# Kernel tuning notes

Hardware: AMD Instinct MI355X
Metric: run time of the kernel (lower is better)

## Reference

```python
import jax, jax.numpy as jnp
import numpy as np

N_NODES = 100000
N_EDGES = 1600000
N_GRAPHS = 128
ATOM_F = 92
BOND_F = 41
EMB = 64
HID = 128
CHG = 16
N_LAYERS = 3
EPS = 1e-5


def setup_inputs() -> dict:
    key = jax.random.key(0)
    ks = jax.random.split(key, 32)
    s = 0.05
    inp = {
        "x": jax.random.normal(ks[0], (N_NODES, ATOM_F), jnp.float32),
        "edge_attr": jax.random.uniform(ks[1], (N_EDGES, BOND_F), jnp.float32),
        "charge": jax.random.normal(ks[2], (N_GRAPHS,), jnp.float32),
        "edge_index": jax.random.randint(ks[3], (2, N_EDGES), 0, N_NODES),
        "batch": jnp.sort(jax.random.randint(ks[4], (N_NODES,), 0, N_GRAPHS)),
        # embeddings
        "W_charge": jax.random.normal(ks[5], (1, CHG), jnp.float32) * s,
        "b_charge": jnp.zeros((CHG,), jnp.float32),
        "W_atom": jax.random.normal(ks[6], (ATOM_F + CHG, EMB), jnp.float32) * s,
        "b_atom": jnp.zeros((EMB,), jnp.float32),
        "W_bond": jax.random.normal(ks[7], (BOND_F, EMB), jnp.float32) * s,
        "b_bond": jnp.zeros((EMB,), jnp.float32),
        # conv layers (stacked over layer dim)
        "conv_eW1": jax.random.normal(ks[8], (N_LAYERS, 3 * EMB, EMB), jnp.float32) * s,
        "conv_eb1": jnp.zeros((N_LAYERS, EMB), jnp.float32),
        "conv_eW2": jax.random.normal(ks[9], (N_LAYERS, EMB, EMB), jnp.float32) * s,
        "conv_eb2": jnp.zeros((N_LAYERS, EMB), jnp.float32),
        "conv_nW1": jax.random.normal(ks[10], (N_LAYERS, 2 * EMB, EMB), jnp.float32) * s,
        "conv_nb1": jnp.zeros((N_LAYERS, EMB), jnp.float32),
        "conv_nW2": jax.random.normal(ks[11], (N_LAYERS, EMB, EMB), jnp.float32) * s,
        "conv_nb2": jnp.zeros((N_LAYERS, EMB), jnp.float32),
        "bn_gamma": jnp.ones((N_LAYERS, EMB), jnp.float32),
        "bn_beta": jnp.zeros((N_LAYERS, EMB), jnp.float32),
        # predictor
        "pW1": jax.random.normal(ks[12], (EMB, HID), jnp.float32) * s,
        "pb1": jnp.zeros((HID,), jnp.float32),
        "pW2": jax.random.normal(ks[13], (HID, HID), jnp.float32) * s,
        "pb2": jnp.zeros((HID,), jnp.float32),
        "pW3": jax.random.normal(ks[14], (HID, 1), jnp.float32) * s,
        "pb3": jnp.zeros((1,), jnp.float32),
    }
    return inp


def reference(x, edge_attr, charge, W_charge, b_charge, W_atom, b_atom,
              W_bond, b_bond, conv_eW1, conv_eb1, conv_eW2, conv_eb2,
              conv_nW1, conv_nb1, conv_nW2, conv_nb2, bn_gamma, bn_beta,
              pW1, pb1, pW2, pb2, pW3, pb3, edge_index, batch):
    sp = jax.nn.softplus
    n_nodes = x.shape[0]
    n_graphs = charge.shape[0]

    # early charge integration: per-graph charge embedding broadcast to nodes
    charge_feat = charge[:, None] @ W_charge + b_charge          # [B, CHG]
    x = jnp.concatenate([x, charge_feat[batch]], axis=1)          # [N, ATOM_F+CHG]
    x = x @ W_atom + b_atom                                       # [N, EMB]
    ea = edge_attr @ W_bond + b_bond                              # [E, EMB]

    row, col = edge_index[0], edge_index[1]
    for i in range(conv_eW1.shape[0]):
        xr, xc = x[row], x[col]                                   # gathers [E, EMB]
        # edge update: MLP on [x_row, x_col, edge_attr]
        e_in = jnp.concatenate([xr, xc, ea], axis=1)              # [E, 3*EMB]
        ea = sp(e_in @ conv_eW1[i] + conv_eb1[i]) @ conv_eW2[i] + conv_eb2[i]
        # node messages: MLP on [x_row, new edge_attr]
        m_in = jnp.concatenate([xr, ea], axis=1)                  # [E, 2*EMB]
        msg = sp(m_in @ conv_nW1[i] + conv_nb1[i]) @ conv_nW2[i] + conv_nb2[i]
        x_new = jax.ops.segment_sum(msg, col, num_segments=n_nodes)
        # BatchNorm1d (training-mode batch stats, biased variance)
        mean = jnp.mean(x_new, axis=0)
        var = jnp.var(x_new, axis=0)
        x_new = (x_new - mean) * jax.lax.rsqrt(var + EPS) * bn_gamma[i] + bn_beta[i]
        x = sp(x_new) + x                                         # residual

    # global mean pool over graphs
    sums = jax.ops.segment_sum(x, batch, num_segments=n_graphs)   # [B, EMB]
    cnt = jax.ops.segment_sum(jnp.ones((n_nodes, 1), x.dtype), batch, num_segments=n_graphs)
    g = sums / jnp.maximum(cnt, 1.0)

    # predictor MLP (dropout is identity in eval mode)
    h = sp(g @ pW1 + pb1)
    h = sp(h @ pW2 + pb2)
    out = h @ pW3 + pb3                                           # [B, 1]
    return out.squeeze(-1)
```

## Files before the change

kernel.cpp:

```cpp
#include <hip/hip_runtime.h>
#include <math.h>

typedef short v8s __attribute__((ext_vector_type(8)));
typedef float v4f __attribute__((ext_vector_type(4)));

__device__ __forceinline__ float sp_f(float x) {
  return fmaxf(x, 0.0f) + 0.69314718056f * __log2f(1.0f + __expf(-fabsf(x)));
}

__device__ __forceinline__ unsigned short f2bf(float f) {
  union { float f; unsigned u; } x; x.f = f;
  unsigned r = (x.u + 0x7FFF + ((x.u >> 16) & 1)) >> 16;
  return (unsigned short)r;
}

__device__ __forceinline__ float bf2f(unsigned short h) {
  union { unsigned u; float f; } x; x.u = ((unsigned)h) << 16;
  return x.f;
}

__global__ __launch_bounds__(256) void k_prep_wfrag(
    const float* __restrict__ eW1, const float* __restrict__ eW2,
    const float* __restrict__ nW1, const float* __restrict__ nW2,
    unsigned short* __restrict__ wfrag) {
  int i = blockIdx.x >> 2;
  int m = blockIdx.x & 3;
  const float* W;
  if (m == 0)      W = eW1 + (size_t)i * 192 * 64 + 128 * 64;
  else if (m == 1) W = eW2 + (size_t)i * 64 * 64;
  else if (m == 2) W = nW1 + (size_t)i * 128 * 64 + 64 * 64;
  else             W = nW2 + (size_t)i * 64 * 64;
  unsigned short* out = wfrag + ((size_t)i * 4 + m) * 4096;
  for (int f = threadIdx.x; f < 4096; f += 256) {
    int j = f & 7, ln = (f >> 3) & 63, kh = (f >> 9) & 1, ct = f >> 10;
    int k = kh * 32 + (ln >> 4) * 8 + j;
    int n = ct * 16 + (ln & 15);
    out[f] = f2bf(W[k * 64 + n]);
  }
}

__global__ __launch_bounds__(256) void k_embed_nodes(
    const float* __restrict__ x, const int* __restrict__ batch,
    const float* __restrict__ charge, const float* __restrict__ W_charge,
    const float* __restrict__ b_charge, const float* __restrict__ W_atom,
    const float* __restrict__ b_atom, float* __restrict__ xemb, int N) {
  __shared__ float sW[108 * 64];
  __shared__ float sX[128 * 92];
  __shared__ float sb[64];
  __shared__ float sWc[16];
  __shared__ float sbc[16];
  for (int i = threadIdx.x; i < 108 * 64; i += blockDim.x) sW[i] = W_atom[i];
  if (threadIdx.x < 64) sb[threadIdx.x] = b_atom[threadIdx.x];
  if (threadIdx.x < 16) {
    sWc[threadIdx.x] = W_charge[threadIdx.x];
    sbc[threadIdx.x] = b_charge[threadIdx.x];
  }
  int ntiles = (N + 127) >> 7;
  for (int tile = blockIdx.x; tile < ntiles; tile += gridDim.x) {
    int base = tile << 7;
    int cnt = N - base; if (cnt > 128) cnt = 128;
    __syncthreads();
    if (cnt == 128) {
      const float4* src = (const float4*)(x + (size_t)base * 92);
      for (int i = threadIdx.x; i < 2944; i += 256) ((float4*)sX)[i] = src[i];
    } else {
      for (int i = threadIdx.x; i < cnt * 92; i += 256)
        sX[i] = x[(size_t)base * 92 + i];
    }
    __syncthreads();
    int t = threadIdx.x;
    int node = t & 127, half = t >> 7;
    if (node < cnt) {
      int n = base + node;
      float acc[32];
#pragma unroll
      for (int j = 0; j < 32; ++j) acc[j] = sb[half * 32 + j];
      const float* xr = sX + node * 92;
      for (int k = 0; k < 92; ++k) {
        float a = xr[k];
        const float* wk = sW + k * 64 + half * 32;
#pragma unroll
        for (int j = 0; j < 32; ++j) acc[j] = fmaf(a, wk[j], acc[j]);
      }
      float ch = charge[batch[n]];
#pragma unroll
      for (int c = 0; c < 16; ++c) {
        float cf = fmaf(ch, sWc[c], sbc[c]);
        const float* wk = sW + (92 + c) * 64 + half * 32;
#pragma unroll
        for (int j = 0; j < 32; ++j) acc[j] = fmaf(cf, wk[j], acc[j]);
      }
      float* o = xemb + (size_t)n * 64 + half * 32;
#pragma unroll
      for (int q8 = 0; q8 < 8; ++q8)
        ((float4*)o)[q8] = make_float4(acc[4*q8], acc[4*q8+1], acc[4*q8+2], acc[4*q8+3]);
    }
  }
}

__global__ __launch_bounds__(256) void k_hist(const int* __restrict__ col,
                                              int* __restrict__ counts, int E) {
  int stride = gridDim.x * blockDim.x;
  for (int e = blockIdx.x * blockDim.x + threadIdx.x; e < E; e += stride)
    atomicAdd(&counts[col[e]], 1);
}

__global__ __launch_bounds__(256) void k_scan1(const int* __restrict__ counts,
                                               int* __restrict__ scan_tmp,
                                               int* __restrict__ bsum, int N) {
  __shared__ int sd[2][256];
  int t = threadIdx.x;
  int i = blockIdx.x * 256 + t;
  int v = (i < N) ? counts[i] : 0;
  sd[0][t] = v;
  __syncthreads();
  int s = 0;
#pragma unroll
  for (int off = 1; off < 256; off <<= 1) {
    int nv = sd[s][t];
    if (t >= off) nv += sd[s][t - off];
    sd[s ^ 1][t] = nv;
    s ^= 1;
    __syncthreads();
  }
  if (i < N) scan_tmp[i] = sd[s][t];
  if (t == 255) bsum[blockIdx.x] = sd[s][255];
}

__global__ __launch_bounds__(256) void k_scan2(int* __restrict__ b, int NB) {
  __shared__ int sd[2][256];
  __shared__ int carry_s;
  int t = threadIdx.x;
  if (t == 0) carry_s = 0;
  __syncthreads();
  for (int base = 0; base < NB; base += 256) {
    int i = base + t;
    int v = (i < NB) ? b[i] : 0;
    sd[0][t] = v;
    __syncthreads();
    int s = 0;
#pragma unroll
    for (int off = 1; off < 256; off <<= 1) {
      int nv = sd[s][t];
      if (t >= off) nv += sd[s][t - off];
      sd[s ^ 1][t] = nv;
      s ^= 1;
      __syncthreads();
    }
    int c = carry_s;
    int tot = sd[s][255];
    if (i < NB) b[i] = sd[s][t] + c;
    __syncthreads();
    if (t == 0) carry_s = c + tot;
    __syncthreads();
  }
}

__global__ __launch_bounds__(256) void k_scan3(const int* __restrict__ counts,
                                               const int* __restrict__ scan_tmp,
                                               const int* __restrict__ bsum,
                                               int* __restrict__ cursor, int N) {
  int i = blockIdx.x * 256 + threadIdx.x;
  if (i < N) {
    int base = (blockIdx.x > 0) ? bsum[blockIdx.x - 1] : 0;
    cursor[i] = scan_tmp[i] - counts[i] + base;
  }
}

__global__ __launch_bounds__(256) void k_scatter(
    const int* __restrict__ row, const int* __restrict__ col,
    int* __restrict__ cursor, int* __restrict__ pos,
    int* __restrict__ row_s, int* __restrict__ col_s, int E) {
  int stride = gridDim.x * blockDim.x;
  for (int e = blockIdx.x * blockDim.x + threadIdx.x; e < E; e += stride) {
    int c = col[e];
    int p = atomicAdd(&cursor[c], 1);
    pos[e] = p;
    row_s[p] = row[e];
    col_s[p] = c;
  }
}

__global__ __launch_bounds__(256) void k_embed_bonds_pos(
    const float* __restrict__ eattr, const int* __restrict__ pos,
    const float* __restrict__ W_bond, const float* __restrict__ b_bond,
    unsigned short* __restrict__ ea16, int E) {
  __shared__ float sW[41 * 64];
  __shared__ float sE[256 * 41];
  __shared__ float sb[64];
  for (int i = threadIdx.x; i < 41 * 64; i += blockDim.x) sW[i] = W_bond[i];
  if (threadIdx.x < 64) sb[threadIdx.x] = b_bond[threadIdx.x];
  int ntiles = (E + 255) >> 8;
  for (int tile = blockIdx.x; tile < ntiles; tile += gridDim.x) {
    int base = tile << 8;
    int cnt = E - base; if (cnt > 256) cnt = 256;
    __syncthreads();
    if (cnt == 256) {
      const float4* src = (const float4*)(eattr + (size_t)base * 41);
      for (int i = threadIdx.x; i < 2624; i += 256) ((float4*)sE)[i] = src[i];
    } else {
      for (int i = threadIdx.x; i < cnt * 41; i += 256)
        sE[i] = eattr[(size_t)base * 41 + i];
    }
    __syncthreads();
    int t = threadIdx.x;
    if (t < cnt) {
      float acc[64];
#pragma unroll
      for (int j = 0; j < 64; ++j) acc[j] = sb[j];
      const float* er = sE + t * 41;
      for (int k = 0; k < 41; ++k) {
        float a = er[k];
        const float* wk = sW + k * 64;
#pragma unroll
        for (int j = 0; j < 64; ++j) acc[j] = fmaf(a, wk[j], acc[j]);
      }
      size_t ob = (size_t)pos[base + t] * 64;
#pragma unroll
      for (int q8 = 0; q8 < 8; ++q8) {
        unsigned short tmp[8];
#pragma unroll
        for (int j = 0; j < 8; ++j) tmp[j] = f2bf(acc[q8 * 8 + j]);
        *(uint4*)&ea16[ob + q8 * 8] = *(uint4*)tmp;
      }
    }
  }
}

__device__ __forceinline__ void node_pre_body(
    const float* __restrict__ xr, const float* sWa, const float* sWb,
    const float* sWp, unsigned short* __restrict__ up16,
    unsigned short* __restrict__ v16, int n) {
  const float4* xr4 = (const float4*)xr;
  float u[64], p[64];
#pragma unroll
  for (int j = 0; j < 64; ++j) { u[j] = 0.f; p[j] = 0.f; }
  for (int k4 = 0; k4 < 16; ++k4) {
    float4 av = xr4[k4];
    const float* wa = sWa + k4 * 256;
    const float* wp = sWp + k4 * 256;
#pragma unroll
    for (int j = 0; j < 64; ++j) u[j] = fmaf(av.x, wa[j], u[j]);
#pragma unroll
    for (int j = 0; j < 64; ++j) p[j] = fmaf(av.x, wp[j], p[j]);
#pragma unroll
    for (int j = 0; j < 64; ++j) u[j] = fmaf(av.y, wa[64 + j], u[j]);
#pragma unroll
    for (int j = 0; j < 64; ++j) p[j] = fmaf(av.y, wp[64 + j], p[j]);
#pragma unroll
    for (int j = 0; j < 64; ++j) u[j] = fmaf(av.z, wa[128 + j], u[j]);
#pragma unroll
    for (int j = 0; j < 64; ++j) p[j] = fmaf(av.z, wp[128 + j], p[j]);
#pragma unroll
    for (int j = 0; j < 64; ++j) u[j] = fmaf(av.w, wa[192 + j], u[j]);
#pragma unroll
    for (int j = 0; j < 64; ++j) p[j] = fmaf(av.w, wp[192 + j], p[j]);
  }
  unsigned short* o = up16 + (size_t)n * 128;
#pragma unroll
  for (int q8 = 0; q8 < 8; ++q8) {
    unsigned short tmp[8];
#pragma unroll
    for (int j = 0; j < 8; ++j) {
      int i = q8 * 8 + j;
      tmp[j] = f2bf(u[((i & 3) << 4) | (i >> 2)]);
    }
    *(uint4*)&o[q8 * 8] = *(uint4*)tmp;
  }
#pragma unroll
  for (int q8 = 0; q8 < 8; ++q8) {
    unsigned short tmp[8];
#pragma unroll
    for (int j = 0; j < 8; ++j) {
      int i = q8 * 8 + j;
      tmp[j] = f2bf(p[((i & 3) << 4) | (i >> 2)]);
    }
    *(uint4*)&o[64 + q8 * 8] = *(uint4*)tmp;
  }
  float vv[64];
#pragma unroll
  for (int j = 0; j < 64; ++j) vv[j] = 0.f;
  for (int k4 = 0; k4 < 16; ++k4) {
    float4 av = xr4[k4];
    const float* wb = sWb + k4 * 256;
#pragma unroll
    for (int j = 0; j < 64; ++j) vv[j] = fmaf(av.x, wb[j], vv[j]);
#pragma unroll
    for (int j = 0; j < 64; ++j) vv[j] = fmaf(av.y, wb[64 + j], vv[j]);
#pragma unroll
    for (int j = 0; j < 64; ++j) vv[j] = fmaf(av.z, wb[128 + j], vv[j]);
#pragma unroll
    for (int j = 0; j < 64; ++j) vv[j] = fmaf(av.w, wb[192 + j], vv[j]);
  }
  unsigned short* ov = v16 + (size_t)n * 64;
#pragma unroll
  for (int q8 = 0; q8 < 8; ++q8) {
    unsigned short tmp[8];
#pragma unroll
    for (int j = 0; j < 8; ++j) {
      int i = q8 * 8 + j;
      tmp[j] = f2bf(vv[((i & 3) << 4) | (i >> 2)]);
    }
    *(uint4*)&ov[q8 * 8] = *(uint4*)tmp;
  }
}

__global__ __launch_bounds__(256) void k_node_pre(
    const float* __restrict__ xemb, const float* __restrict__ eW1,
    const float* __restrict__ nW1, unsigned short* __restrict__ up16,
    unsigned short* __restrict__ v16, int N) {
  __shared__ float sWa[64 * 64];
  __shared__ float sWb[64 * 64];
  __shared__ float sWp[64 * 64];
  for (int i = threadIdx.x; i < 64 * 64; i += blockDim.x) {
    sWa[i] = eW1[i];
    sWb[i] = eW1[64 * 64 + i];
    sWp[i] = nW1[i];
  }
  __syncthreads();
  int stride = gridDim.x * blockDim.x;
  for (int n = blockIdx.x * blockDim.x + threadIdx.x; n < N; n += stride)
    node_pre_body(xemb + (size_t)n * 64, sWa, sWb, sWp, up16, v16, n);
}

__global__ __launch_bounds__(256) void k_bn_pre(
    float* __restrict__ xemb, const float* __restrict__ xnew,
    const float* __restrict__ bnacc, const float* __restrict__ gamma,
    const float* __restrict__ beta, const float* __restrict__ eW1n,
    const float* __restrict__ nW1n, unsigned short* __restrict__ up16,
    unsigned short* __restrict__ v16, int N) {
  __shared__ float sWa[64 * 64];
  __shared__ float sWb[64 * 64];
  __shared__ float sWp[64 * 64];
  __shared__ float sscale[64], sshift[64];
  for (int i = threadIdx.x; i < 64 * 64; i += blockDim.x) {
    sWa[i] = eW1n[i];
    sWb[i] = eW1n[64 * 64 + i];
    sWp[i] = nW1n[i];
  }
  if (threadIdx.x < 64) {
    float inv = 1.0f / (float)N;
    float m = bnacc[threadIdx.x] * inv;
    float var = bnacc[64 + threadIdx.x] * inv - m * m;
    float rs = rsqrtf(var + 1e-5f);
    float g = gamma[threadIdx.x];
    sscale[threadIdx.x] = rs * g;
    sshift[threadIdx.x] = beta[threadIdx.x] - m * rs * g;
  }
  __syncthreads();
  int stride = gridDim.x * blockDim.x;
  for (int n = blockIdx.x * blockDim.x + threadIdx.x; n < N; n += stride) {
    float* xr = xemb + (size_t)n * 64;
#pragma unroll
    for (int q = 0; q < 16; ++q) {
      float4 xn4 = ((const float4*)(xnew + (size_t)n * 64))[q];
      float4 xo4 = ((const float4*)xr)[q];
      xo4.x += sp_f(fmaf(xn4.x, sscale[4*q+0], sshift[4*q+0]));
      xo4.y += sp_f(fmaf(xn4.y, sscale[4*q+1], sshift[4*q+1]));
      xo4.z += sp_f(fmaf(xn4.z, sscale[4*q+2], sshift[4*q+2]));
      xo4.w += sp_f(fmaf(xn4.w, sscale[4*q+3], sshift[4*q+3]));
      ((float4*)xr)[q] = xo4;
    }
    node_pre_body(xr, sWa, sWb, sWp, up16, v16, n);
  }
}

#define READ_FRAGS(P)                                                        \
  {                                                                          \
    const v8s* wp_ = (const v8s*)gWf + (P) * 512;                            \
    _Pragma("unroll") for (int ct = 0; ct < 4; ++ct)                         \
        _Pragma("unroll") for (int kh = 0; kh < 2; ++kh)                     \
            bfr[ct][kh] = wp_[(ct * 2 + kh) * 64 + l];                       \
    _Pragma("unroll") for (int rb = 0; rb < 2; ++rb)                         \
        _Pragma("unroll") for (int kh = 0; kh < 2; ++kh) {                   \
      int row_ = rbase + rb * 16 + c16;                                      \
      af[rb][kh] = *(const v8s*)&sA[row_ * 64 +                              \
                                    ((kh * 32 + q * 8) ^ ((row_ & 7) << 3))];\
    }                                                                        \
  }

#define DO_MFMA()                                                            \
  _Pragma("unroll") for (int rb = 0; rb < 2; ++rb)                           \
      _Pragma("unroll") for (int ct = 0; ct < 4; ++ct) {                     \
    v4f a_ = {0.f, 0.f, 0.f, 0.f};                                           \
    a_ = __builtin_amdgcn_mfma_f32_16x16x32_bf16(af[rb][0], bfr[ct][0], a_,  \
                                                 0, 0, 0);                   \
    a_ = __builtin_amdgcn_mfma_f32_16x16x32_bf16(af[rb][1], bfr[ct][1], a_,  \
                                                 0, 0, 0);                   \
    acc[rb][ct] = a_;                                                        \
  }

__global__ __launch_bounds__(256, 4) void k_edge_mfma(
    const int* __restrict__ row_s, const int* __restrict__ col_s,
    unsigned short* __restrict__ ea16, const unsigned short* __restrict__ up16,
    const unsigned short* __restrict__ v16,
    const unsigned short* __restrict__ gWf, const float* __restrict__ eb1,
    const float* __restrict__ eb2, const float* __restrict__ nb1,
    const float* __restrict__ nb2, float* __restrict__ xnew, int E) {
  __shared__ __align__(16) unsigned char smem[34304];
  unsigned short* sA = (unsigned short*)smem;
  float* msgb        = (float*)smem;
  float* sBb         = (float*)(smem + 32768);
  int* scol          = (int*)(smem + 33792);

  int tid = threadIdx.x;
  int te = blockIdx.x * 128;
  int w = tid >> 6, l = tid & 63, q = l >> 4, c16 = l & 15;
  int rbase = w * 32;

  int rid[2][4], cid[2][4], eid[2][4];
#pragma unroll
  for (int rb = 0; rb < 2; ++rb)
#pragma unroll
    for (int r = 0; r < 4; ++r) {
      int rit = rbase + rb * 16 + q * 4 + r;
      int e = te + rit;
      eid[rb][r] = e;
      int ec = e < E ? e : E - 1;
      rid[rb][r] = row_s[ec];
      cid[rb][r] = col_s[ec];
    }
  ushort4 uu_pf[2][4], vv_pf[2][4];
#pragma unroll
  for (int rb = 0; rb < 2; ++rb)
#pragma unroll
    for (int r = 0; r < 4; ++r) {
      uu_pf[rb][r] = *(const ushort4*)&up16[(size_t)rid[rb][r] * 128 + c16 * 4];
      vv_pf[rb][r] = *(const ushort4*)&v16[(size_t)cid[rb][r] * 64 + c16 * 4];
    }

  if (tid < 64) {
    sBb[0 * 64 + tid] = eb1[tid];
    sBb[1 * 64 + tid] = eb2[tid];
    sBb[2 * 64 + tid] = nb1[tid];
    sBb[3 * 64 + tid] = nb2[tid];
  }
  if (tid < 128) {
    int e = te + tid;
    scol[tid] = col_s[e < E ? e : E - 1];
  }
  for (int i = tid; i < 1024; i += 256) {
    int r = i >> 3, cc = i & 7;
    int e = te + r;
    if (e >= E) e = E - 1;
    uint4 d = *(const uint4*)&ea16[(size_t)e * 64 + cc * 8];
    *(uint4*)&sA[r * 64 + ((cc * 8) ^ ((r & 7) << 3))] = d;
  }

  v8s af[2][2];
  v8s bfr[4][2];
  v4f acc[2][4];

  __syncthreads();

  READ_FRAGS(0);
  DO_MFMA();
  ushort4 pp_pf[2][4];
#pragma unroll
  for (int rb = 0; rb < 2; ++rb)
#pragma unroll
    for (int r = 0; r < 4; ++r)
      pp_pf[rb][r] =
          *(const ushort4*)&up16[(size_t)rid[rb][r] * 128 + 64 + c16 * 4];
#pragma unroll
  for (int rb = 0; rb < 2; ++rb)
#pragma unroll
    for (int r = 0; r < 4; ++r) {
      int row = rbase + rb * 16 + q * 4 + r;
      const unsigned short* up_ = (const unsigned short*)&uu_pf[rb][r];
      const unsigned short* vp_ = (const unsigned short*)&vv_pf[rb][r];
#pragma unroll
      for (int ct = 0; ct < 4; ++ct) {
        int n = ct * 16 + c16;
        float t = acc[rb][ct][r] + sBb[n] + bf2f(up_[ct]) + bf2f(vp_[ct]);
        t = sp_f(t);
        sA[row * 64 + (n ^ ((row & 7) << 3))] = f2bf(t);
      }
    }

  READ_FRAGS(1);
  DO_MFMA();
#pragma unroll
  for (int rb = 0; rb < 2; ++rb)
#pragma unroll
    for (int ct = 0; ct < 4; ++ct) {
      int n = ct * 16 + c16;
#pragma unroll
      for (int r = 0; r < 4; ++r) {
        float en = acc[rb][ct][r] + sBb[64 + n];
        int row = rbase + rb * 16 + q * 4 + r;
        sA[row * 64 + (n ^ ((row & 7) << 3))] = f2bf(en);
      }
    }
  __syncthreads();
  for (int i = tid; i < 1024; i += 256) {
    int r = i >> 3, cc = i & 7;
    if (te + r < E) {
      uint4 d = *(const uint4*)&sA[r * 64 + ((cc * 8) ^ ((r & 7) << 3))];
      *(uint4*)&ea16[(size_t)(te + r) * 64 + cc * 8] = d;
    }
  }
  __syncthreads();

  READ_FRAGS(2);
  DO_MFMA();
#pragma unroll
  for (int rb = 0; rb < 2; ++rb)
#pragma unroll
    for (int r = 0; r < 4; ++r) {
      int row = rbase + rb * 16 + q * 4 + r;
      const unsigned short* pp_ = (const unsigned short*)&pp_pf[rb][r];
#pragma unroll
      for (int ct = 0; ct < 4; ++ct) {
        int n = ct * 16 + c16;
        float t2 = acc[rb][ct][r] + sBb[128 + n] + bf2f(pp_[ct]);
        t2 = sp_f(t2);
        sA[row * 64 + (n ^ ((row & 7) << 3))] = f2bf(t2);
      }
    }

  READ_FRAGS(3);
  __syncthreads();
  DO_MFMA();
#pragma unroll
  for (int rb = 0; rb < 2; ++rb)
#pragma unroll
    for (int ct = 0; ct < 4; ++ct) {
      int n = ct * 16 + c16;
#pragma unroll
      for (int r = 0; r < 4; ++r) {
        float msg = acc[rb][ct][r] + sBb[192 + n];
        int row = rbase + rb * 16 + q * 4 + r;
        msgb[row * 64 + n] = (eid[rb][r] < E) ? msg : 0.0f;
      }
    }
  __syncthreads();

  int nrows = E - te;
  if (nrows > 128) nrows = 128;
  for (int r0 = w; r0 < nrows; r0 += 4) {
    int c0 = scol[r0];
    if (r0 > 0 && scol[r0 - 1] == c0) continue;
    float s = 0.0f;
    int r = r0;
    do {
      s += msgb[r * 64 + l];
      ++r;
    } while (r < nrows && scol[r] == c0);
    atomicAdd(&xnew[(size_t)c0 * 64 + l], s);
  }
}

__global__ __launch_bounds__(256) void k_bn_stats(
    const float* __restrict__ xnew, float* __restrict__ bnacc, int N) {
  int t = threadIdx.x;
  int ch = t & 63;
  int sl = t >> 6;
  float s = 0.f, s2 = 0.f;
  for (int n = blockIdx.x * 4 + sl; n < N; n += gridDim.x * 4) {
    float v = xnew[(size_t)n * 64 + ch];
    s += v;
    s2 = fmaf(v, v, s2);
  }
  __shared__ float red[256], red2[256];
  red[t] = s;
  red2[t] = s2;
  __syncthreads();
  if (sl == 0) {
    s = red[ch] + red[64 + ch] + red[128 + ch] + red[192 + ch];
    s2 = red2[ch] + red2[64 + ch] + red2[128 + ch] + red2[192 + ch];
    atomicAdd(&bnacc[ch], s);
    atomicAdd(&bnacc[64 + ch], s2);
  }
}

__global__ __launch_bounds__(256) void k_bn_apply(
    float* __restrict__ x, const float* __restrict__ xnew,
    const float* __restrict__ bnacc, const float* __restrict__ gamma,
    const float* __restrict__ beta, int N) {
  __shared__ float sscale[64], sshift[64];
  if (threadIdx.x < 64) {
    float inv = 1.0f / (float)N;
    float m = bnacc[threadIdx.x] * inv;
    float var = bnacc[64 + threadIdx.x] * inv - m * m;
    float rs = rsqrtf(var + 1e-5f);
    float g = gamma[threadIdx.x];
    sscale[threadIdx.x] = rs * g;
    sshift[threadIdx.x] = beta[threadIdx.x] - m * rs * g;
  }
  __syncthreads();
  size_t total = (size_t)N * 64;
  size_t stride = (size_t)gridDim.x * blockDim.x;
  for (size_t i = (size_t)blockIdx.x * blockDim.x + threadIdx.x; i < total; i += stride) {
    int ch = (int)(i & 63);
    float v = fmaf(xnew[i], sscale[ch], sshift[ch]);
    x[i] += sp_f(v);
  }
}

__device__ __forceinline__ int lbound(const int* a, int n, int key) {
  int lo = 0, hi = n;
  while (lo < hi) {
    int mid = (lo + hi) >> 1;
    if (a[mid] < key) lo = mid + 1; else hi = mid;
  }
  return lo;
}

__global__ __launch_bounds__(256) void k_pool_pred(
    const float* __restrict__ x, const int* __restrict__ batch, int N,
    const float* __restrict__ pW1, const float* __restrict__ pb1,
    const float* __restrict__ pW2, const float* __restrict__ pb2,
    const float* __restrict__ pW3, const float* __restrict__ pb3,
    float* __restrict__ out) {
  int b = blockIdx.x;
  int lo = lbound(batch, N, b);
  int hi = lbound(batch, N, b + 1);
  int t = threadIdx.x;
  int ch = t & 63;
  int sl = t >> 6;
  float s = 0.f;
  for (int n = lo + sl; n < hi; n += 4) s += x[(size_t)n * 64 + ch];
  __shared__ float red4[4][64];
  __shared__ float sg[64];
  __shared__ float sh1[128];
  __shared__ float red[128];
  red4[sl][ch] = s;
  __syncthreads();
  if (t < 64) {
    float tot = red4[0][t] + red4[1][t] + red4[2][t] + red4[3][t];
    float cnt = (float)(hi - lo);
    sg[t] = tot / fmaxf(cnt, 1.0f);
  }
  __syncthreads();
  if (t < 128) {
    float h = pb1[t];
    for (int k = 0; k < 64; ++k) h = fmaf(sg[k], pW1[k * 128 + t], h);
    sh1[t] = sp_f(h);
  }
  __syncthreads();
  if (t < 128) {
    float h = pb2[t];
    for (int k = 0; k < 128; ++k) h = fmaf(sh1[k], pW2[k * 128 + t], h);
    red[t] = sp_f(h) * pW3[t];
  }
  __syncthreads();
  for (int off = 64; off > 0; off >>= 1) {
    if (t < off) red[t] += red[t + off];
    __syncthreads();
  }
  if (t == 0) out[b] = red[0] + pb3[0];
}

extern "C" void kernel_launch(void* const* d_in, const int* in_sizes, int n_in,
                              void* d_out, int out_size, void* d_ws, size_t ws_size,
                              hipStream_t stream) {
  const float* x         = (const float*)d_in[0];
  const float* edge_attr = (const float*)d_in[1];
  const float* charge    = (const float*)d_in[2];
  const int*   eidx      = (const int*)d_in[3];
  const int*   batch     = (const int*)d_in[4];
  const float* W_charge  = (const float*)d_in[5];
  const float* b_charge  = (const float*)d_in[6];
  const float* W_atom    = (const float*)d_in[7];
  const float* b_atom    = (const float*)d_in[8];
  const float* W_bond    = (const float*)d_in[9];
  const float* b_bond    = (const float*)d_in[10];
  const float* eW1 = (const float*)d_in[11];
  const float* eb1 = (const float*)d_in[12];
  const float* eW2 = (const float*)d_in[13];
  const float* eb2 = (const float*)d_in[14];
  const float* nW1 = (const float*)d_in[15];
  const float* nb1 = (const float*)d_in[16];
  const float* nW2 = (const float*)d_in[17];
  const float* nb2 = (const float*)d_in[18];
  const float* gam = (const float*)d_in[19];
  const float* bet = (const float*)d_in[20];
  const float* pW1 = (const float*)d_in[21];
  const float* pb1 = (const float*)d_in[22];
  const float* pW2 = (const float*)d_in[23];
  const float* pb2 = (const float*)d_in[24];
  const float* pW3 = (const float*)d_in[25];
  const float* pb3 = (const float*)d_in[26];

  int N = in_sizes[4];
  int E = in_sizes[3] / 2;
  int B = in_sizes[2];
  const int* row = eidx;
  const int* col = eidx + E;

  char* wptr = (char*)d_ws;
  unsigned short* ea16 = (unsigned short*)wptr; wptr += (((size_t)E * 64 * 2 + 255) & ~255ull);
  unsigned short* up16 = (unsigned short*)wptr; wptr += (((size_t)N * 128 * 2 + 255) & ~255ull);
  unsigned short* v16  = (unsigned short*)wptr; wptr += (((size_t)N * 64 * 2 + 255) & ~255ull);
  unsigned short* wfrag = (unsigned short*)wptr; wptr += 12 * 4096 * 2;
  float* xemb = (float*)wptr; wptr += (size_t)N * 64 * 4;
  float* xnew = (float*)wptr; wptr += (size_t)N * 64 * 4;
  float* bnacc = (float*)wptr; wptr += 256 * 4;
  int* counts = (int*)wptr;   wptr += (size_t)N * 4;
  int* scan_tmp = (int*)wptr; wptr += (size_t)N * 4;
  int* cursor = (int*)wptr;   wptr += (size_t)N * 4;
  int* bsum = (int*)wptr;     wptr += 4096;
  int* pos = (int*)wptr;      wptr += (size_t)E * 4;
  int* row_s = (int*)wptr;    wptr += (size_t)E * 4;
  int* col_s = (int*)wptr;    wptr += (size_t)E * 4;

  int NB = (N + 255) / 256;

  k_prep_wfrag<<<12, 256, 0, stream>>>(eW1, eW2, nW1, nW2, wfrag);
  hipMemsetAsync(counts, 0, (size_t)N * 4, stream);
  k_hist<<<2048, 256, 0, stream>>>(col, counts, E);
  k_scan1<<<NB, 256, 0, stream>>>(counts, scan_tmp, bsum, N);
  k_scan2<<<1, 256, 0, stream>>>(bsum, NB);
  k_scan3<<<NB, 256, 0, stream>>>(counts, scan_tmp, bsum, cursor, N);
  k_scatter<<<2048, 256, 0, stream>>>(row, col, cursor, pos, row_s, col_s, E);

  int ntilesN = (N + 127) / 128;
  k_embed_nodes<<<ntilesN, 256, 0, stream>>>(x, batch, charge, W_charge,
                                             b_charge, W_atom, b_atom, xemb, N);
  k_embed_bonds_pos<<<2048, 256, 0, stream>>>(edge_attr, pos, W_bond, b_bond,
                                              ea16, E);
  k_node_pre<<<NB, 256, 0, stream>>>(xemb, eW1, nW1, up16, v16, N);

  int gridE = (E + 127) / 128;
  for (int i = 0; i < 3; ++i) {
    hipMemsetAsync(xnew, 0, (size_t)N * 64 * 4, stream);
    hipMemsetAsync(bnacc, 0, 256 * 4, stream);
    k_edge_mfma<<<gridE, 256, 0, stream>>>(
        row_s, col_s, ea16, up16, v16, wfrag + (size_t)i * 16384,
        eb1 + (size_t)i * 64, eb2 + (size_t)i * 64, nb1 + (size_t)i * 64,
        nb2 + (size_t)i * 64, xnew, E);
    k_bn_stats<<<1024, 256, 0, stream>>>(xnew, bnacc, N);
    if (i < 2) {
      k_bn_pre<<<NB, 256, 0, stream>>>(
          xemb, xnew, bnacc, gam + (size_t)i * 64, bet + (size_t)i * 64,
          eW1 + (size_t)(i + 1) * 192 * 64, nW1 + (size_t)(i + 1) * 128 * 64,
          up16, v16, N);
    } else {
      k_bn_apply<<<4096, 256, 0, stream>>>(xemb, xnew, bnacc,
                                           gam + (size_t)i * 64,
                                           bet + (size_t)i * 64, N);
    }
  }

  k_pool_pred<<<B, 256, 0, stream>>>(xemb, batch, N, pW1, pb1, pW2, pb2,
                                     pW3, pb3, (float*)d_out);
}
```

Baseline: 2.198 ms.

## Use 512-thread edge blocks, skip last-layer edge store, replace interior atomics

Measured after the change: 2.200 ms. No clear change (+0.1%).

```diff
diff --git a/kernel.cpp b/kernel.cpp
--- a/kernel.cpp
+++ b/kernel.cpp
@@ -371,32 +371,32 @@
     _Pragma("unroll") for (int ct = 0; ct < 4; ++ct)                         \
         _Pragma("unroll") for (int kh = 0; kh < 2; ++kh)                     \
             bfr[ct][kh] = wp_[(ct * 2 + kh) * 64 + l];                       \
-    _Pragma("unroll") for (int rb = 0; rb < 2; ++rb)                         \
-        _Pragma("unroll") for (int kh = 0; kh < 2; ++kh) {                   \
-      int row_ = rbase + rb * 16 + c16;                                      \
-      af[rb][kh] = *(const v8s*)&sA[row_ * 64 +                              \
-                                    ((kh * 32 + q * 8) ^ ((row_ & 7) << 3))];\
+    {                                                                        \
+      int row_ = rbase + c16;                                                \
+      _Pragma("unroll") for (int kh = 0; kh < 2; ++kh)                       \
+        af[kh] = *(const v8s*)&sA[row_ * 64 +                                \
+                                  ((kh * 32 + q * 8) ^ ((row_ & 7) << 3))];  \
     }                                                                        \
   }
 
 #define DO_MFMA()                                                            \
-  _Pragma("unroll") for (int rb = 0; rb < 2; ++rb)                           \
-      _Pragma("unroll") for (int ct = 0; ct < 4; ++ct) {                     \
+  _Pragma("unroll") for (int ct = 0; ct < 4; ++ct) {                         \
     v4f a_ = {0.f, 0.f, 0.f, 0.f};                                           \
-    a_ = __builtin_amdgcn_mfma_f32_16x16x32_bf16(af[rb][0], bfr[ct][0], a_,  \
+    a_ = __builtin_amdgcn_mfma_f32_16x16x32_bf16(af[0], bfr[ct][0], a_,      \
                                                  0, 0, 0);                   \
-    a_ = __builtin_amdgcn_mfma_f32_16x16x32_bf16(af[rb][1], bfr[ct][1], a_,  \
+    a_ = __builtin_amdgcn_mfma_f32_16x16x32_bf16(af[1], bfr[ct][1], a_,      \
                                                  0, 0, 0);                   \
-    acc[rb][ct] = a_;                                                        \
-  }
-
-__global__ __launch_bounds__(256, 4) void k_edge_mfma(
+    acc[ct] = a_;                                                            \
+  }
+
+__global__ __launch_bounds__(512, 8) void k_edge_mfma(
     const int* __restrict__ row_s, const int* __restrict__ col_s,
     unsigned short* __restrict__ ea16, const unsigned short* __restrict__ up16,
     const unsigned short* __restrict__ v16,
     const unsigned short* __restrict__ gWf, const float* __restrict__ eb1,
     const float* __restrict__ eb2, const float* __restrict__ nb1,
-    const float* __restrict__ nb2, float* __restrict__ xnew, int E) {
+    const float* __restrict__ nb2, float* __restrict__ xnew, int E,
+    int store_ea) {
   __shared__ __align__(16) unsigned char smem[34304];
   unsigned short* sA = (unsigned short*)smem;
   float* msgb        = (float*)smem;
@@ -406,28 +406,17 @@
   int tid = threadIdx.x;
   int te = blockIdx.x * 128;
   int w = tid >> 6, l = tid & 63, q = l >> 4, c16 = l & 15;
-  int rbase = w * 32;
-
-  int rid[2][4], cid[2][4], eid[2][4];
-#pragma unroll
-  for (int rb = 0; rb < 2; ++rb)
-#pragma unroll
-    for (int r = 0; r < 4; ++r) {
-      int rit = rbase + rb * 16 + q * 4 + r;
-      int e = te + rit;
-      eid[rb][r] = e;
-      int ec = e < E ? e : E - 1;
-      rid[rb][r] = row_s[ec];
-      cid[rb][r] = col_s[ec];
-    }
-  ushort4 uu_pf[2][4], vv_pf[2][4];
-#pragma unroll
-  for (int rb = 0; rb < 2; ++rb)
-#pragma unroll
-    for (int r = 0; r < 4; ++r) {
-      uu_pf[rb][r] = *(const ushort4*)&up16[(size_t)rid[rb][r] * 128 + c16 * 4];
-      vv_pf[rb][r] = *(const ushort4*)&v16[(size_t)cid[rb][r] * 64 + c16 * 4];
-    }
+  int rbase = w * 16;
+
+  int rid[4], cid[4], eid[4];
+#pragma unroll
+  for (int r = 0; r < 4; ++r) {
+    int e = te + rbase + q * 4 + r;
+    eid[r] = e;
+    int ec = e < E ? e : E - 1;
+    rid[r] = row_s[ec];
+    cid[r] = col_s[ec];
+  }
 
   if (tid < 64) {
     sBb[0 * 64 + tid] = eb1[tid];
@@ -439,7 +428,7 @@
     int e = te + tid;
     scol[tid] = col_s[e < E ? e : E - 1];
   }
-  for (int i = tid; i < 1024; i += 256) {
+  for (int i = tid; i < 1024; i += 512) {
     int r = i >> 3, cc = i & 7;
     int e = te + r;
     if (e >= E) e = E - 1;
@@ -447,98 +436,88 @@
     *(uint4*)&sA[r * 64 + ((cc * 8) ^ ((r & 7) << 3))] = d;
   }
 
-  v8s af[2][2];
+  v8s af[2];
   v8s bfr[4][2];
-  v4f acc[2][4];
+  v4f acc[4];
 
   __syncthreads();
 
   READ_FRAGS(0);
   DO_MFMA();
-  ushort4 pp_pf[2][4];
-#pragma unroll
-  for (int rb = 0; rb < 2; ++rb)
-#pragma unroll
-    for (int r = 0; r < 4; ++r)
-      pp_pf[rb][r] =
-          *(const ushort4*)&up16[(size_t)rid[rb][r] * 128 + 64 + c16 * 4];
-#pragma unroll
-  for (int rb = 0; rb < 2; ++rb)
-#pragma unroll
-    for (int r = 0; r < 4; ++r) {
-      int row = rbase + rb * 16 + q * 4 + r;
-      const unsigned short* up_ = (const unsigned short*)&uu_pf[rb][r];
-      const unsigned short* vp_ = (const unsigned short*)&vv_pf[rb][r];
-#pragma unroll
-      for (int ct = 0; ct < 4; ++ct) {
-        int n = ct * 16 + c16;
-        float t = acc[rb][ct][r] + sBb[n] + bf2f(up_[ct]) + bf2f(vp_[ct]);
-        t = sp_f(t);
-        sA[row * 64 + (n ^ ((row & 7) << 3))] = f2bf(t);
-      }
-    }
+#pragma unroll
+  for (int r = 0; r < 4; ++r) {
+    ushort4 uu = *(const ushort4*)&up16[(size_t)rid[r] * 128 + c16 * 4];
+    ushort4 vv = *(const ushort4*)&v16[(size_t)cid[r] * 64 + c16 * 4];
+    int row = rbase + q * 4 + r;
+    const unsigned short* up_ = (const unsigned short*)&uu;
+    const unsigned short* vp_ = (const unsigned short*)&vv;
+#pragma unroll
+    for (int ct = 0; ct < 4; ++ct) {
+      int n = ct * 16 + c16;
+      float t = acc[ct][r] + sBb[n] + bf2f(up_[ct]) + bf2f(vp_[ct]);
+      t = sp_f(t);
+      sA[row * 64 + (n ^ ((row & 7) << 3))] = f2bf(t);
+    }
+  }
 
   READ_FRAGS(1);
   DO_MFMA();
 #pragma unroll
-  for (int rb = 0; rb < 2; ++rb)
+  for (int ct = 0; ct < 4; ++ct) {
+    int n = ct * 16 + c16;
+#pragma unroll
+    for (int r = 0; r < 4; ++r) {
+      float en = acc[ct][r] + sBb[64 + n];
+      int row = rbase + q * 4 + r;
+      sA[row * 64 + (n ^ ((row & 7) << 3))] = f2bf(en);
+    }
+  }
+  __syncthreads();
+  if (store_ea) {
+    for (int i = tid; i < 1024; i += 512) {
+      int r = i >> 3, cc = i & 7;
+      if (te + r < E) {
+        uint4 d = *(const uint4*)&sA[r * 64 + ((cc * 8) ^ ((r & 7) << 3))];
+        *(uint4*)&ea16[(size_t)(te + r) * 64 + cc * 8] = d;
+      }
+    }
+  }
+  __syncthreads();
+
+  READ_FRAGS(2);
+  DO_MFMA();
+#pragma unroll
+  for (int r = 0; r < 4; ++r) {
+    ushort4 pp = *(const ushort4*)&up16[(size_t)rid[r] * 128 + 64 + c16 * 4];
+    int row = rbase + q * 4 + r;
+    const unsigned short* pp_ = (const unsigned short*)&pp;
 #pragma unroll
     for (int ct = 0; ct < 4; ++ct) {
       int n = ct * 16 + c16;
-#pragma unroll
-      for (int r = 0; r < 4; ++r) {
-        float en = acc[rb][ct][r] + sBb[64 + n];
-        int row = rbase + rb * 16 + q * 4 + r;
-        sA[row * 64 + (n ^ ((row & 7) << 3))] = f2bf(en);
-      }
-    }
-  __syncthreads();
-  for (int i = tid; i < 1024; i += 256) {
-    int r = i >> 3, cc = i & 7;
-    if (te + r < E) {
-      uint4 d = *(const uint4*)&sA[r * 64 + ((cc * 8) ^ ((r & 7) << 3))];
-      *(uint4*)&ea16[(size_t)(te + r) * 64 + cc * 8] = d;
-    }
-  }
-  __syncthreads();
-
-  READ_FRAGS(2);
+      float t2 = acc[ct][r] + sBb[128 + n] + bf2f(pp_[ct]);
+      t2 = sp_f(t2);
+      sA[row * 64 + (n ^ ((row & 7) << 3))] = f2bf(t2);
+    }
+  }
+
+  READ_FRAGS(3);
+  __syncthreads();
   DO_MFMA();
 #pragma unroll
-  for (int rb = 0; rb < 2; ++rb)
+  for (int ct = 0; ct < 4; ++ct) {
+    int n = ct * 16 + c16;
 #pragma unroll
     for (int r = 0; r < 4; ++r) {
-      int row = rbase + rb * 16 + q * 4 + r;
-      const unsigned short* pp_ = (const unsigned short*)&pp_pf[rb][r];
-#pragma unroll
-      for (int ct = 0; ct < 4; ++ct) {
-        int n = ct * 16 + c16;
-        float t2 = acc[rb][ct][r] + sBb[128 + n] + bf2f(pp_[ct]);
-        t2 = sp_f(t2);
-        sA[row * 64 + (n ^ ((row & 7) << 3))] = f2bf(t2);
-      }
-    }
-
-  READ_FRAGS(3);
-  __syncthreads();
-  DO_MFMA();
-#pragma unroll
-  for (int rb = 0; rb < 2; ++rb)
-#pragma unroll
-    for (int ct = 0; ct < 4; ++ct) {
-      int n = ct * 16 + c16;
-#pragma unroll
-      for (int r = 0; r < 4; ++r) {
-        float msg = acc[rb][ct][r] + sBb[192 + n];
-        int row = rbase + rb * 16 + q * 4 + r;
-        msgb[row * 64 + n] = (eid[rb][r] < E) ? msg : 0.0f;
-      }
-    }
+      float msg = acc[ct][r] + sBb[192 + n];
+      int row = rbase + q * 4 + r;
+      msgb[row * 64 + n] = (eid[r] < E) ? msg : 0.0f;
+    }
+  }
   __syncthreads();
 
   int nrows = E - te;
   if (nrows > 128) nrows = 128;
-  for (int r0 = w; r0 < nrows; r0 += 4) {
+  for (int r0 = w; r0 < nrows; r0 += 8) {
     int c0 = scol[r0];
     if (r0 > 0 && scol[r0 - 1] == c0) continue;
     float s = 0.0f;
@@ -547,7 +526,10 @@
       s += msgb[r * 64 + l];
       ++r;
     } while (r < nrows && scol[r] == c0);
-    atomicAdd(&xnew[(size_t)c0 * 64 + l], s);
+    if (r0 > 0 && r < nrows)
+      xnew[(size_t)c0 * 64 + l] = s;
+    else
+      atomicAdd(&xnew[(size_t)c0 * 64 + l], s);
   }
 }
 
@@ -726,10 +708,10 @@
   for (int i = 0; i < 3; ++i) {
     hipMemsetAsync(xnew, 0, (size_t)N * 64 * 4, stream);
     hipMemsetAsync(bnacc, 0, 256 * 4, stream);
-    k_edge_mfma<<<gridE, 256, 0, stream>>>(
+    k_edge_mfma<<<gridE, 512, 0, stream>>>(
         row_s, col_s, ea16, up16, v16, wfrag + (size_t)i * 16384,
         eb1 + (size_t)i * 64, eb2 + (size_t)i * 64, nb1 + (size_t)i * 64,
-        nb2 + (size_t)i * 64, xnew, E);
+        nb2 + (size_t)i * 64, xnew, E, (i < 2) ? 1 : 0);
     k_bn_stats<<<1024, 256, 0, stream>>>(xnew, bnacc, N);
     if (i < 2) {
       k_bn_pre<<<NB, 256, 0, stream>>>(
```
